# Optimization experiments

Measured on AMD Instinct MI355X. Metric: run time of the kernel, lower is better.

The kernel has to match this reference:

```python
import jax, jax.numpy as jnp
import numpy as np
from math import comb

# Implicit Bernstein form (BERN-NN-Implicit): a polynomial in V vars is a stack of
# term blocks; each term = V rows of univariate Bernstein coefficients, poly value
# = sum over terms of the product over vars of the univariate Bernstein polys.
N_IN, T_IN, V, DEG = 16, 64, 4, 4
C = DEG + 1          # coeffs per row at degree DEG
K = 2 * DEG + 1      # coeffs per row at degree 2*DEG (after squaring)

def _prod_matrix(d):
    # Bernstein product: (deg d) x (deg d) -> deg 2d ; c_k = sum_{i+j=k} b_i b_j C(d,i)C(d,j)/C(2d,k)
    M = np.zeros((d + 1, d + 1, 2 * d + 1), np.float32)
    for i in range(d + 1):
        for j in range(d + 1):
            M[i, j, i + j] = comb(d, i) * comb(d, j) / comb(2 * d, i + j)
    return jnp.asarray(M)

def _elev_matrix(d):
    # degree elevation d -> 2d : b'_j = sum_i b_i C(d,i)C(d,j-i)/C(2d,j)
    E = np.zeros((d + 1, 2 * d + 1), np.float32)
    for i in range(d + 1):
        for j in range(i, i + d + 1):
            E[i, j] = comb(d, i) * comb(d, j - i) / comb(2 * d, j)
    return jnp.asarray(E)

M_PROD = _prod_matrix(DEG)
E_ELEV = _elev_matrix(DEG)

def _scaled_terms(polys, w, idx):
    # mult_with_constant fused over all contributing inputs: scale row 0 of each term
    # block by the (nonzero) weight; concat of term blocks == sum_2_polys at equal degree.
    if idx.size == 0:
        return jnp.zeros((1, V, C), polys.dtype)  # zero polynomial (one zero term)
    sel = polys[idx]                                   # (n, T, V, C)
    sel = sel.at[:, :, 0, :].multiply(w[idx][:, None, None])
    return sel.reshape(-1, V, C)

def _add_const(P, c):
    # add_with_constant: append a constant term (Bernstein coeffs of a constant are all c)
    cols = P.shape[-1]
    row0 = c * jnp.ones((1, 1, cols), P.dtype)
    rest = jnp.ones((1, V - 1, cols), P.dtype)
    return jnp.concatenate([P, jnp.concatenate([row0, rest], axis=1)], axis=0)

def _ibf_minmax(P):
    # per-term interval = product over vars of [min,max] of each row; sum over terms
    lo = P.min(axis=-1); hi = P.max(axis=-1)           # (T, V)
    tlo, thi = lo[:, 0], hi[:, 0]
    for v in range(1, V):
        cands = jnp.stack([tlo * lo[:, v], tlo * hi[:, v], thi * lo[:, v], thi * hi[:, v]])
        tlo, thi = cands.min(0), cands.max(0)
    return tlo.sum(), thi.sum()

def _quad_of_poly(P, a, b, c):
    # a*p^2 + b*p + c in implicit Bernstein form; p^2 = all pairwise term products
    T = P.shape[0]
    sq = jnp.einsum('avi,bvj,ijk->abvk', P, P, M_PROD).reshape(T * T, V, K)
    sq = sq.at[:, 0, :].multiply(a)
    lin = jnp.einsum('tvi,ij->tvj', P, E_ELEV)          # elevate DEG -> 2*DEG
    lin = lin.at[:, 0, :].multiply(b)
    const = jnp.concatenate([c * jnp.ones((1, 1, K)), jnp.ones((1, V - 1, K))], axis=1)
    return jnp.concatenate([sq, lin, const], axis=0)

def _node_io(under_in, over_in, pos_w, neg_w, bias, pos_idx, neg_idx):
    under = jnp.concatenate([_scaled_terms(over_in, neg_w, neg_idx),
                             _scaled_terms(under_in, pos_w, pos_idx)], axis=0)
    under = _add_const(under, bias)
    over = jnp.concatenate([_scaled_terms(over_in, pos_w, pos_idx),
                            _scaled_terms(under_in, neg_w, neg_idx)], axis=0)
    over = _add_const(over, bias)
    return under, over

def setup_inputs() -> dict:
    key = jax.random.key(0)
    k1, k2, k3 = jax.random.split(key, 3)
    ui = 0.5 * jax.random.normal(k1, (N_IN, T_IN, V, C), jnp.float32)
    oi = ui + 0.05 * jnp.abs(jax.random.normal(k2, (N_IN, T_IN, V, C), jnp.float32))
    w = jax.random.normal(k3, (N_IN,), jnp.float32)
    return {
        'layer_inputs_under': ui,
        'layer_inputs_over': oi,
        'node_pos_weights': jnp.maximum(w, 0.0),
        'node_neg_weights': jnp.minimum(w, 0.0),
        'node_bias': jnp.asarray(-0.1, jnp.float32),
        'layer_inputs_under_degrees': jnp.full((N_IN, V), DEG, jnp.int32),
        'layer_inputs_over_degrees': jnp.full((N_IN, V), DEG, jnp.int32),
    }

def reference(layer_inputs_under, layer_inputs_over, node_pos_weights, node_neg_weights,
              node_bias, layer_inputs_under_degrees, layer_inputs_over_degrees):
    pos_idx = np.nonzero(np.asarray(node_pos_weights))[0]
    neg_idx = np.nonzero(np.asarray(node_neg_weights))[0]
    under, over = _node_io(layer_inputs_under, layer_inputs_over,
                           node_pos_weights, node_neg_weights, node_bias, pos_idx, neg_idx)
    deg = jnp.maximum(layer_inputs_under_degrees.astype(jnp.float32).max(0),
                      layer_inputs_over_degrees.astype(jnp.float32).max(0))  # (V,)
    l = _ibf_minmax(under)[0]
    u = _ibf_minmax(over)[1]
    lf, uf = float(l), float(u)   # host sync, mirrors the original's data-dependent branch
    if uf <= 0.0:
        return (jnp.zeros((1,)), jnp.zeros((1,)), jnp.zeros(V), jnp.zeros(V))
    if lf >= 0.0:
        return (under.reshape(-1, C), over.reshape(-1, C), deg, deg)
    # mixed case: sound quadratic relaxation of ReLU on [l, u]
    a, b, c = 1.0 / (-4.0 * l), 0.5, -l / 4.0   # upper: (x - l)^2 / (-4 l) >= relu(x)
    over_q = _quad_of_poly(over, a, b, c).reshape(-1, K)
    if uf >= -lf:
        # under relaxation = identity (coeffs [0,1,0])
        return (under.reshape(-1, C), over_q, deg, 2.0 * deg)
    # under relaxation = 0 (coeffs all zero)
    return (jnp.zeros((V, 1)), over_q, jnp.zeros(V), 2.0 * deg)
```

## Files before the change

### kernel.cpp

```cpp
#include <hip/hip_runtime.h>

#define NINP 16
#define TIN 64
#define NV 4
#define NC 5
#define NK 9
#define T_ROWS 1025
#define NPAIR (1025 * 1025)
#define UNDER_SZ (T_ROWS * NV * NC)
#define OQ_OFF UNDER_SZ
#define OQ_SQ_SZ (NPAIR * NV * NK)
#define TAIL_ELEMS ((T_ROWS + 1) * NV * NK)
#define DEG_OFF (OQ_OFF + OQ_SQ_SZ + TAIL_ELEMS)
#define WS_POVER 0
#define WS_L 20500

__device__ __forceinline__ int count_nz16(const float* __restrict__ w) {
    int c = 0;
#pragma unroll
    for (int n = 0; n < NINP; n++) c += (w[n] != 0.0f) ? 1 : 0;
    return c;
}

__device__ __forceinline__ int kth_nz16(const float* __restrict__ w, int k) {
    int c = 0, r = 0;
#pragma unroll
    for (int n = 0; n < NINP; n++) {
        bool nz = (w[n] != 0.0f);
        if (nz && c == k) r = n;
        c += nz ? 1 : 0;
    }
    return r;
}

__global__ void prep_kernel(const float* __restrict__ ui, const float* __restrict__ oi,
                            const float* __restrict__ posw, const float* __restrict__ negw,
                            const float* __restrict__ bias,
                            const int* __restrict__ udeg, const int* __restrict__ odeg,
                            float* __restrict__ out, float* __restrict__ ws) {
    int gid = blockIdx.x * blockDim.x + threadIdx.x;
    if (gid < NV) {
        int m = 0;
        for (int n = 0; n < NINP; n++) {
            int a = udeg[n * NV + gid];
            int b = odeg[n * NV + gid];
            m = max(m, max(a, b));
        }
        out[DEG_OFF + gid] = (float)m;
        out[DEG_OFF + NV + gid] = 2.0f * (float)m;
    }
    if (gid < UNDER_SZ) {
        int r = gid / 20, rem = gid - r * 20, v = rem / 5, c = rem - v * 5;
        float val;
        if (r < 1024) {
            int g = r >> 6, t = r & 63;
            int nNeg = count_nz16(negw);
            if (g < nNeg) {
                int n = kth_nz16(negw, g);
                val = oi[((n * TIN + t) * NV + v) * NC + c] * ((v == 0) ? negw[n] : 1.0f);
            } else {
                int n = kth_nz16(posw, g - nNeg);
                val = ui[((n * TIN + t) * NV + v) * NC + c] * ((v == 0) ? posw[n] : 1.0f);
            }
        } else {
            val = (v == 0) ? bias[0] : 1.0f;
        }
        out[gid] = val;
    } else if (gid < 2 * UNDER_SZ) {
        int e = gid - UNDER_SZ;
        int r = e / 20, rem = e - r * 20, v = rem / 5, c = rem - v * 5;
        float val;
        if (r < 1024) {
            int g = r >> 6, t = r & 63;
            int nPos = count_nz16(posw);
            if (g < nPos) {
                int n = kth_nz16(posw, g);
                val = oi[((n * TIN + t) * NV + v) * NC + c] * ((v == 0) ? posw[n] : 1.0f);
            } else {
                int n = kth_nz16(negw, g - nPos);
                val = ui[((n * TIN + t) * NV + v) * NC + c] * ((v == 0) ? negw[n] : 1.0f);
            }
        } else {
            val = (v == 0) ? bias[0] : 1.0f;
        }
        ws[WS_POVER + e] = val;
    }
}

__device__ __forceinline__ float row_lower(const float* __restrict__ P, int r) {
    const float* row = P + r * 20;
    float tlo = 0.f, thi = 0.f;
#pragma unroll
    for (int v = 0; v < NV; v++) {
        float lo = row[v * 5], hi = lo;
#pragma unroll
        for (int c = 1; c < 5; c++) {
            float x = row[v * 5 + c];
            lo = fminf(lo, x);
            hi = fmaxf(hi, x);
        }
        if (v == 0) {
            tlo = lo; thi = hi;
        } else {
            float p0 = tlo * lo, p1 = tlo * hi, p2 = thi * lo, p3 = thi * hi;
            tlo = fminf(fminf(p0, p1), fminf(p2, p3));
            thi = fmaxf(fmaxf(p0, p1), fmaxf(p2, p3));
        }
    }
    return tlo;
}

__global__ __launch_bounds__(1024) void reduce_l_kernel(const float* __restrict__ under,
                                                        float* __restrict__ ws) {
    __shared__ float s[1024];
    int t = threadIdx.x;
    float acc = row_lower(under, t);
    if (t == 0) acc += row_lower(under, 1024);
    s[t] = acc;
    __syncthreads();
    for (int off = 512; off > 0; off >>= 1) {
        if (t < off) s[t] += s[t + off];
        __syncthreads();
    }
    if (t == 0) ws[WS_L] = s[0];
}

__global__ __launch_bounds__(256) void sq_kernel(const float* __restrict__ P,
                                                 const float* __restrict__ lptr,
                                                 float* __restrict__ out) {
    __shared__ float lds[256 * 37];
    const int t = threadIdx.x;
    const int p0 = blockIdx.x * 256;
    int nvalid = NPAIR - p0;
    if (nvalid > 256) nvalid = 256;
    const float l = lptr[0];
    const float ascale = -0.25f / l;

    if (t < nvalid) {
        int p = p0 + t;
        int ai = p / 1025;
        int bi = p - ai * 1025;
        float pa[20], pb[20];
        const float4* A4 = reinterpret_cast<const float4*>(P + ai * 20);
        const float4* B4 = reinterpret_cast<const float4*>(P + bi * 20);
#pragma unroll
        for (int q = 0; q < 5; q++) {
            float4 x = A4[q];
            pa[4 * q] = x.x; pa[4 * q + 1] = x.y; pa[4 * q + 2] = x.z; pa[4 * q + 3] = x.w;
            float4 y = B4[q];
            pb[4 * q] = y.x; pb[4 * q + 1] = y.y; pb[4 * q + 2] = y.z; pb[4 * q + 3] = y.w;
        }
        const float C4[5] = {1.f, 4.f, 6.f, 4.f, 1.f};
        const float invC8[9] = {1.f, 0.125f, 1.f / 28.f, 1.f / 56.f, 1.f / 70.f,
                                1.f / 56.f, 1.f / 28.f, 0.125f, 1.f};
#pragma unroll
        for (int v = 0; v < NV; v++) {
            float a_[5], b_[5];
#pragma unroll
            for (int i = 0; i < 5; i++) {
                a_[i] = pa[v * 5 + i] * C4[i];
                b_[i] = pb[v * 5 + i] * C4[i];
            }
            float cc[9];
#pragma unroll
            for (int k = 0; k < 9; k++) cc[k] = 0.f;
#pragma unroll
            for (int i = 0; i < 5; i++)
#pragma unroll
                for (int j = 0; j < 5; j++) cc[i + j] += a_[i] * b_[j];
            const float sc = (v == 0) ? ascale : 1.0f;
#pragma unroll
            for (int k = 0; k < 9; k++) lds[t * 37 + v * 9 + k] = cc[k] * invC8[k] * sc;
        }
    }
    __syncthreads();

    const int nflt = nvalid * 36;
    const long base = (long)OQ_OFF + (long)p0 * 36;
    int f = t;
    int pl = f / 36, w = f - pl * 36;
    for (; f < nflt; f += 256) {
        out[base + f] = lds[pl * 37 + w];
        pl += 7; w += 4;
        if (w >= 36) { w -= 36; pl++; }
    }
}

__device__ __forceinline__ float c4_of(int j) {
    if (j == 0 || j == 4) return 1.f;
    if (j == 1 || j == 3) return 4.f;
    if (j == 2) return 6.f;
    return 0.f;
}

__global__ void tail_kernel(const float* __restrict__ P, const float* __restrict__ lptr,
                            float* __restrict__ out) {
    int idx = blockIdx.x * blockDim.x + threadIdx.x;
    if (idx >= TAIL_ELEMS) return;
    int rl = idx / 36, rem = idx - rl * 36, v = rem / 9, k = rem - v * 9;
    const float invC8[9] = {1.f, 0.125f, 1.f / 28.f, 1.f / 56.f, 1.f / 70.f,
                            1.f / 56.f, 1.f / 28.f, 0.125f, 1.f};
    const float C4[5] = {1.f, 4.f, 6.f, 4.f, 1.f};
    float val;
    if (rl < T_ROWS) {
        float acc = 0.f;
#pragma unroll
        for (int i = 0; i < 5; i++) {
            float e = C4[i] * c4_of(k - i);
            acc += P[rl * 20 + v * 5 + i] * e;
        }
        val = acc * invC8[k] * ((v == 0) ? 0.5f : 1.0f);
    } else {
        val = (v == 0) ? (-0.25f * lptr[0]) : 1.0f;
    }
    out[OQ_OFF + (long)NPAIR * 36 + idx] = val;
}

extern "C" void kernel_launch(void* const* d_in, const int* in_sizes, int n_in,
                              void* d_out, int out_size, void* d_ws, size_t ws_size,
                              hipStream_t stream) {
    const float* ui   = (const float*)d_in[0];
    const float* oi   = (const float*)d_in[1];
    const float* posw = (const float*)d_in[2];
    const float* negw = (const float*)d_in[3];
    const float* bias = (const float*)d_in[4];
    const int*   udeg = (const int*)d_in[5];
    const int*   odeg = (const int*)d_in[6];
    float* out = (float*)d_out;
    float* ws  = (float*)d_ws;

    prep_kernel<<<(2 * UNDER_SZ + 255) / 256, 256, 0, stream>>>(ui, oi, posw, negw, bias,
                                                                udeg, odeg, out, ws);
    reduce_l_kernel<<<1, 1024, 0, stream>>>(out, ws);
    sq_kernel<<<(NPAIR + 255) / 256, 256, 0, stream>>>(ws + WS_POVER, ws + WS_L, out);
    tail_kernel<<<(TAIL_ELEMS + 255) / 256, 256, 0, stream>>>(ws + WS_POVER, ws + WS_L, out);
}
```

Baseline: 42.03 us.

## Fuse l-reduction into prep and merge square/tail into one kernel

Removes the single-block reduce kernel. Extra prep blocks recompute the under-row lower bounds straight from the inputs and write fixed-point int64 partial sums. The square and tail kernels merge into one launch that sums the partials itself, and the square results are written as float4 stores instead of scalar stores. This cuts two launches and the serial 1024-thread reduction. The fixed-point sum at 2^24 scale can lose precision or overflow for large bounds.

```diff
diff --git a/kernel.cpp b/kernel.cpp
--- a/kernel.cpp
+++ b/kernel.cpp
@@ -13,7 +13,13 @@
 #define TAIL_ELEMS ((T_ROWS + 1) * NV * NK)
 #define DEG_OFF (OQ_OFF + OQ_SQ_SZ + TAIL_ELEMS)
 #define WS_POVER 0
-#define WS_L 20500
+#define L_PART_LL 10252
+#define FIXED_SCALE 16777216.0f
+
+#define PREP_ELEM_BLOCKS 161
+#define PREP_L_BLOCKS 4
+#define PAIR_BLOCKS 4105
+#define TAIL_BLOCKS 145
 
 __device__ __forceinline__ int count_nz16(const float* __restrict__ w) {
     int c = 0;
@@ -33,156 +39,99 @@
     return r;
 }
 
-__global__ void prep_kernel(const float* __restrict__ ui, const float* __restrict__ oi,
-                            const float* __restrict__ posw, const float* __restrict__ negw,
-                            const float* __restrict__ bias,
-                            const int* __restrict__ udeg, const int* __restrict__ odeg,
-                            float* __restrict__ out, float* __restrict__ ws) {
-    int gid = blockIdx.x * blockDim.x + threadIdx.x;
-    if (gid < NV) {
-        int m = 0;
-        for (int n = 0; n < NINP; n++) {
-            int a = udeg[n * NV + gid];
-            int b = odeg[n * NV + gid];
-            m = max(m, max(a, b));
-        }
-        out[DEG_OFF + gid] = (float)m;
-        out[DEG_OFF + NV + gid] = 2.0f * (float)m;
-    }
-    if (gid < UNDER_SZ) {
-        int r = gid / 20, rem = gid - r * 20, v = rem / 5, c = rem - v * 5;
-        float val;
-        if (r < 1024) {
-            int g = r >> 6, t = r & 63;
-            int nNeg = count_nz16(negw);
-            if (g < nNeg) {
-                int n = kth_nz16(negw, g);
-                val = oi[((n * TIN + t) * NV + v) * NC + c] * ((v == 0) ? negw[n] : 1.0f);
+__device__ __forceinline__ float under_val(const float* __restrict__ ui,
+                                           const float* __restrict__ oi,
+                                           const float* __restrict__ posw,
+                                           const float* __restrict__ negw,
+                                           float bias, int r, int v, int c) {
+    if (r < 1024) {
+        int g = r >> 6, tt = r & 63;
+        int nNeg = count_nz16(negw);
+        if (g < nNeg) {
+            int n = kth_nz16(negw, g);
+            return oi[((n * TIN + tt) * NV + v) * NC + c] * ((v == 0) ? negw[n] : 1.0f);
+        }
+        int n = kth_nz16(posw, g - nNeg);
+        return ui[((n * TIN + tt) * NV + v) * NC + c] * ((v == 0) ? posw[n] : 1.0f);
+    }
+    return (v == 0) ? bias : 1.0f;
+}
+
+__global__ __launch_bounds__(256) void prep_kernel(
+    const float* __restrict__ ui, const float* __restrict__ oi,
+    const float* __restrict__ posw, const float* __restrict__ negw,
+    const float* __restrict__ bias,
+    const int* __restrict__ udeg, const int* __restrict__ odeg,
+    float* __restrict__ out, float* __restrict__ ws) {
+    const int bid = blockIdx.x;
+    const int t = threadIdx.x;
+
+    if (bid < PREP_ELEM_BLOCKS) {
+        int gid = bid * 256 + t;
+        if (gid < NV) {
+            int m = 0;
+            for (int n = 0; n < NINP; n++) {
+                int a = udeg[n * NV + gid];
+                int b = odeg[n * NV + gid];
+                m = max(m, max(a, b));
+            }
+            out[DEG_OFF + gid] = (float)m;
+            out[DEG_OFF + NV + gid] = 2.0f * (float)m;
+        }
+        if (gid < UNDER_SZ) {
+            int r = gid / 20, rem = gid - r * 20, v = rem / 5, c = rem - v * 5;
+            out[gid] = under_val(ui, oi, posw, negw, bias[0], r, v, c);
+        } else if (gid < 2 * UNDER_SZ) {
+            int e = gid - UNDER_SZ;
+            int r = e / 20, rem = e - r * 20, v = rem / 5, c = rem - v * 5;
+            float val;
+            if (r < 1024) {
+                int g = r >> 6, tt = r & 63;
+                int nPos = count_nz16(posw);
+                if (g < nPos) {
+                    int n = kth_nz16(posw, g);
+                    val = oi[((n * TIN + tt) * NV + v) * NC + c] * ((v == 0) ? posw[n] : 1.0f);
+                } else {
+                    int n = kth_nz16(negw, g - nPos);
+                    val = ui[((n * TIN + tt) * NV + v) * NC + c] * ((v == 0) ? negw[n] : 1.0f);
+                }
             } else {
-                int n = kth_nz16(posw, g - nNeg);
-                val = ui[((n * TIN + t) * NV + v) * NC + c] * ((v == 0) ? posw[n] : 1.0f);
-            }
-        } else {
-            val = (v == 0) ? bias[0] : 1.0f;
-        }
-        out[gid] = val;
-    } else if (gid < 2 * UNDER_SZ) {
-        int e = gid - UNDER_SZ;
-        int r = e / 20, rem = e - r * 20, v = rem / 5, c = rem - v * 5;
-        float val;
-        if (r < 1024) {
-            int g = r >> 6, t = r & 63;
-            int nPos = count_nz16(posw);
-            if (g < nPos) {
-                int n = kth_nz16(posw, g);
-                val = oi[((n * TIN + t) * NV + v) * NC + c] * ((v == 0) ? posw[n] : 1.0f);
-            } else {
-                int n = kth_nz16(negw, g - nPos);
-                val = ui[((n * TIN + t) * NV + v) * NC + c] * ((v == 0) ? negw[n] : 1.0f);
-            }
-        } else {
-            val = (v == 0) ? bias[0] : 1.0f;
-        }
-        ws[WS_POVER + e] = val;
-    }
-}
-
-__device__ __forceinline__ float row_lower(const float* __restrict__ P, int r) {
-    const float* row = P + r * 20;
-    float tlo = 0.f, thi = 0.f;
-#pragma unroll
-    for (int v = 0; v < NV; v++) {
-        float lo = row[v * 5], hi = lo;
-#pragma unroll
-        for (int c = 1; c < 5; c++) {
-            float x = row[v * 5 + c];
-            lo = fminf(lo, x);
-            hi = fmaxf(hi, x);
-        }
-        if (v == 0) {
-            tlo = lo; thi = hi;
-        } else {
-            float p0 = tlo * lo, p1 = tlo * hi, p2 = thi * lo, p3 = thi * hi;
-            tlo = fminf(fminf(p0, p1), fminf(p2, p3));
-            thi = fmaxf(fmaxf(p0, p1), fmaxf(p2, p3));
-        }
-    }
-    return tlo;
-}
-
-__global__ __launch_bounds__(1024) void reduce_l_kernel(const float* __restrict__ under,
-                                                        float* __restrict__ ws) {
-    __shared__ float s[1024];
-    int t = threadIdx.x;
-    float acc = row_lower(under, t);
-    if (t == 0) acc += row_lower(under, 1024);
-    s[t] = acc;
-    __syncthreads();
-    for (int off = 512; off > 0; off >>= 1) {
-        if (t < off) s[t] += s[t + off];
+                val = (v == 0) ? bias[0] : 1.0f;
+            }
+            ws[WS_POVER + e] = val;
+        }
+    } else {
+        __shared__ long long s[256];
+        const float b0 = bias[0];
+        int r = (bid - PREP_ELEM_BLOCKS) * 256 + t;
+        float tlo = 0.f, thi = 0.f;
+#pragma unroll
+        for (int v = 0; v < NV; v++) {
+            float lo = under_val(ui, oi, posw, negw, b0, r, v, 0), hi = lo;
+#pragma unroll
+            for (int c = 1; c < NC; c++) {
+                float x = under_val(ui, oi, posw, negw, b0, r, v, c);
+                lo = fminf(lo, x);
+                hi = fmaxf(hi, x);
+            }
+            if (v == 0) { tlo = lo; thi = hi; }
+            else {
+                float p0 = tlo * lo, p1 = tlo * hi, p2 = thi * lo, p3 = thi * hi;
+                tlo = fminf(fminf(p0, p1), fminf(p2, p3));
+                thi = fmaxf(fmaxf(p0, p1), fmaxf(p2, p3));
+            }
+        }
+        long long acc = __float2ll_rn(tlo * FIXED_SCALE);
+        if (bid == PREP_ELEM_BLOCKS && t == 0) {
+            acc += __float2ll_rn(b0 * FIXED_SCALE);
+        }
+        s[t] = acc;
         __syncthreads();
-    }
-    if (t == 0) ws[WS_L] = s[0];
-}
-
-__global__ __launch_bounds__(256) void sq_kernel(const float* __restrict__ P,
-                                                 const float* __restrict__ lptr,
-                                                 float* __restrict__ out) {
-    __shared__ float lds[256 * 37];
-    const int t = threadIdx.x;
-    const int p0 = blockIdx.x * 256;
-    int nvalid = NPAIR - p0;
-    if (nvalid > 256) nvalid = 256;
-    const float l = lptr[0];
-    const float ascale = -0.25f / l;
-
-    if (t < nvalid) {
-        int p = p0 + t;
-        int ai = p / 1025;
-        int bi = p - ai * 1025;
-        float pa[20], pb[20];
-        const float4* A4 = reinterpret_cast<const float4*>(P + ai * 20);
-        const float4* B4 = reinterpret_cast<const float4*>(P + bi * 20);
-#pragma unroll
-        for (int q = 0; q < 5; q++) {
-            float4 x = A4[q];
-            pa[4 * q] = x.x; pa[4 * q + 1] = x.y; pa[4 * q + 2] = x.z; pa[4 * q + 3] = x.w;
-            float4 y = B4[q];
-            pb[4 * q] = y.x; pb[4 * q + 1] = y.y; pb[4 * q + 2] = y.z; pb[4 * q + 3] = y.w;
-        }
-        const float C4[5] = {1.f, 4.f, 6.f, 4.f, 1.f};
-        const float invC8[9] = {1.f, 0.125f, 1.f / 28.f, 1.f / 56.f, 1.f / 70.f,
-                                1.f / 56.f, 1.f / 28.f, 0.125f, 1.f};
-#pragma unroll
-        for (int v = 0; v < NV; v++) {
-            float a_[5], b_[5];
-#pragma unroll
-            for (int i = 0; i < 5; i++) {
-                a_[i] = pa[v * 5 + i] * C4[i];
-                b_[i] = pb[v * 5 + i] * C4[i];
-            }
-            float cc[9];
-#pragma unroll
-            for (int k = 0; k < 9; k++) cc[k] = 0.f;
-#pragma unroll
-            for (int i = 0; i < 5; i++)
-#pragma unroll
-                for (int j = 0; j < 5; j++) cc[i + j] += a_[i] * b_[j];
-            const float sc = (v == 0) ? ascale : 1.0f;
-#pragma unroll
-            for (int k = 0; k < 9; k++) lds[t * 37 + v * 9 + k] = cc[k] * invC8[k] * sc;
-        }
-    }
-    __syncthreads();
-
-    const int nflt = nvalid * 36;
-    const long base = (long)OQ_OFF + (long)p0 * 36;
-    int f = t;
-    int pl = f / 36, w = f - pl * 36;
-    for (; f < nflt; f += 256) {
-        out[base + f] = lds[pl * 37 + w];
-        pl += 7; w += 4;
-        if (w >= 36) { w -= 36; pl++; }
+        for (int off = 128; off > 0; off >>= 1) {
+            if (t < off) s[t] += s[t + off];
+            __syncthreads();
+        }
+        if (t == 0) ((long long*)ws)[L_PART_LL + (bid - PREP_ELEM_BLOCKS)] = s[0];
     }
 }
 
@@ -193,27 +142,95 @@
     return 0.f;
 }
 
-__global__ void tail_kernel(const float* __restrict__ P, const float* __restrict__ lptr,
-                            float* __restrict__ out) {
-    int idx = blockIdx.x * blockDim.x + threadIdx.x;
-    if (idx >= TAIL_ELEMS) return;
-    int rl = idx / 36, rem = idx - rl * 36, v = rem / 9, k = rem - v * 9;
-    const float invC8[9] = {1.f, 0.125f, 1.f / 28.f, 1.f / 56.f, 1.f / 70.f,
-                            1.f / 56.f, 1.f / 28.f, 0.125f, 1.f};
-    const float C4[5] = {1.f, 4.f, 6.f, 4.f, 1.f};
-    float val;
-    if (rl < T_ROWS) {
-        float acc = 0.f;
-#pragma unroll
-        for (int i = 0; i < 5; i++) {
-            float e = C4[i] * c4_of(k - i);
-            acc += P[rl * 20 + v * 5 + i] * e;
-        }
-        val = acc * invC8[k] * ((v == 0) ? 0.5f : 1.0f);
+__global__ __launch_bounds__(256) void main_kernel(const float* __restrict__ P,
+                                                   const long long* __restrict__ lpart,
+                                                   float* __restrict__ out) {
+    const int bid = blockIdx.x;
+    const int t = threadIdx.x;
+    const long long ll = lpart[0] + lpart[1] + lpart[2] + lpart[3];
+    const float l = (float)ll * (1.0f / FIXED_SCALE);
+
+    if (bid < PAIR_BLOCKS) {
+        __shared__ float lds[256 * 37];
+        const int p0 = bid * 256;
+        int nvalid = NPAIR - p0;
+        if (nvalid > 256) nvalid = 256;
+        const float ascale = -0.25f / l;
+
+        if (t < nvalid) {
+            int p = p0 + t;
+            int ai = p / 1025;
+            int bi = p - ai * 1025;
+            float pa[20], pb[20];
+            const float4* A4 = reinterpret_cast<const float4*>(P + ai * 20);
+            const float4* B4 = reinterpret_cast<const float4*>(P + bi * 20);
+#pragma unroll
+            for (int q = 0; q < 5; q++) {
+                float4 x = A4[q];
+                pa[4 * q] = x.x; pa[4 * q + 1] = x.y; pa[4 * q + 2] = x.z; pa[4 * q + 3] = x.w;
+                float4 y = B4[q];
+                pb[4 * q] = y.x; pb[4 * q + 1] = y.y; pb[4 * q + 2] = y.z; pb[4 * q + 3] = y.w;
+            }
+            const float C4[5] = {1.f, 4.f, 6.f, 4.f, 1.f};
+            const float invC8[9] = {1.f, 0.125f, 1.f / 28.f, 1.f / 56.f, 1.f / 70.f,
+                                    1.f / 56.f, 1.f / 28.f, 0.125f, 1.f};
+#pragma unroll
+            for (int v = 0; v < NV; v++) {
+                float a_[5], b_[5];
+#pragma unroll
+                for (int i = 0; i < 5; i++) {
+                    a_[i] = pa[v * 5 + i] * C4[i];
+                    b_[i] = pb[v * 5 + i] * C4[i];
+                }
+                float cc[9];
+#pragma unroll
+                for (int k = 0; k < 9; k++) cc[k] = 0.f;
+#pragma unroll
+                for (int i = 0; i < 5; i++)
+#pragma unroll
+                    for (int j = 0; j < 5; j++) cc[i + j] += a_[i] * b_[j];
+                const float sc = (v == 0) ? ascale : 1.0f;
+#pragma unroll
+                for (int k = 0; k < 9; k++) lds[t * 37 + v * 9 + k] = cc[k] * invC8[k] * sc;
+            }
+        }
+        __syncthreads();
+
+        const int nf4 = nvalid * 9;
+        float4* out4 = reinterpret_cast<float4*>(out) + (5125 + (long)p0 * 9);
+        int f4 = t;
+        int pl = t / 9, w4 = (t % 9) * 4;
+        for (; f4 < nf4; f4 += 256) {
+            float4 r;
+            r.x = lds[pl * 37 + w4];
+            r.y = lds[pl * 37 + w4 + 1];
+            r.z = lds[pl * 37 + w4 + 2];
+            r.w = lds[pl * 37 + w4 + 3];
+            out4[f4] = r;
+            pl += 28; w4 += 16;
+            if (w4 >= 36) { w4 -= 36; pl++; }
+        }
     } else {
-        val = (v == 0) ? (-0.25f * lptr[0]) : 1.0f;
-    }
-    out[OQ_OFF + (long)NPAIR * 36 + idx] = val;
+        int idx = (bid - PAIR_BLOCKS) * 256 + t;
+        if (idx >= TAIL_ELEMS) return;
+        int rl = idx / 36, rem = idx - rl * 36, v = rem / 9, k = rem - v * 9;
+        const float invC8[9] = {1.f, 0.125f, 1.f / 28.f, 1.f / 56.f, 1.f / 70.f,
+                                1.f / 56.f, 1.f / 28.f, 0.125f, 1.f};
+        const float C4[5] = {1.f, 4.f, 6.f, 4.f, 1.f};
+        float val;
+        if (rl < T_ROWS) {
+            float acc = 0.f;
+#pragma unroll
+            for (int i = 0; i < 5; i++) {
+                float e = C4[i] * c4_of(k - i);
+                acc += P[rl * 20 + v * 5 + i] * e;
+            }
+            val = acc * invC8[k] * ((v == 0) ? 0.5f : 1.0f);
+        } else {
+            val = (v == 0) ? (-0.25f * l) : 1.0f;
+        }
+        out[OQ_OFF + (long)NPAIR * 36 + idx] = val;
+    }
 }
 
 extern "C" void kernel_launch(void* const* d_in, const int* in_sizes, int n_in,
@@ -229,9 +246,8 @@
     float* out = (float*)d_out;
     float* ws  = (float*)d_ws;
 
-    prep_kernel<<<(2 * UNDER_SZ + 255) / 256, 256, 0, stream>>>(ui, oi, posw, negw, bias,
-                                                                udeg, odeg, out, ws);
-    reduce_l_kernel<<<1, 1024, 0, stream>>>(out, ws);
-    sq_kernel<<<(NPAIR + 255) / 256, 256, 0, stream>>>(ws + WS_POVER, ws + WS_L, out);
-    tail_kernel<<<(TAIL_ELEMS + 255) / 256, 256, 0, stream>>>(ws + WS_POVER, ws + WS_L, out);
-}
+    prep_kernel<<<PREP_ELEM_BLOCKS + PREP_L_BLOCKS, 256, 0, stream>>>(
+        ui, oi, posw, negw, bias, udeg, odeg, out, ws);
+    main_kernel<<<PAIR_BLOCKS + TAIL_BLOCKS, 256, 0, stream>>>(
+        ws + WS_POVER, ((const long long*)ws) + L_PART_LL, out);
+}
```

After: 43.81 us. 4.2% more time.
